# Kernel tuning notes

Measured on AMD Instinct MI355X. Metric: run time of the kernel, lower is better.

Reference implementation:

```python
import jax, jax.numpy as jnp
import numpy as np

N = 100000    # nodes
R = 8         # relations
HFR = 128     # input feature dim
HTO = 128     # output feature dim
NNZ = 1600000 # edges (nonzeros of the (N*R, N) sparse matrix)


def setup_inputs() -> dict:
    key = jax.random.key(0)
    k1, k2, k3, k4, k5 = jax.random.split(key, 5)
    nodes = jax.random.normal(k1, (N, HFR), dtype=jnp.float32)
    rows = jax.random.randint(k2, (NNZ,), 0, N * R)   # row index into (N*R, N) sparse matrix
    cols = jax.random.randint(k3, (NNZ,), 0, N)       # column = source node
    indices = jnp.stack([rows, cols]).astype(jnp.int64)
    values = jax.random.uniform(k4, (NNZ,), dtype=jnp.float32)
    # xavier-uniform-ish init for (r, hfr, hto) relation weights
    weights = jax.random.normal(k5, (R, HFR, HTO), dtype=jnp.float32) * np.float32(1.0 / np.sqrt(HFR))
    return {"nodes": nodes, "indices": indices, "values": values, "weights": weights}


def reference(nodes, indices, values, weights):
    # nodes: [n, hfr]; indices: [2, nnz]; values: [nnz]; weights: [r, hfr, hto]
    n = nodes.shape[0]
    r = weights.shape[0]
    rows, cols = indices[0], indices[1]
    # spmm: (n*r, n) sparse @ (n, hfr) dense -> (n*r, hfr)
    msgs = values[:, None] * nodes[cols]                      # [nnz, hfr] gather + scale
    agg = jax.ops.segment_sum(msgs, rows, num_segments=n * r)  # [n*r, hfr] scatter-add
    agg = agg.reshape(r, n, -1)                                # [r, n, hfr]
    # per-relation GEMM 'rij,rnj->nri' followed by sum over r, fused into one einsum
    out = jnp.einsum('rij,rnj->ni', weights, agg)              # [n, hto]
    return jax.nn.relu(out)
```

## Files before the change

### kernel.cpp

```cpp
#include <hip/hip_runtime.h>
#include <hip/hip_bf16.h>
#include <stdint.h>

#define HFR 128
#define HTO 128
#define LDN 136

typedef short short8 __attribute__((ext_vector_type(8)));
typedef float f32x4  __attribute__((ext_vector_type(4)));
typedef unsigned long long u64;

static __device__ __forceinline__ unsigned short f2bf(float x) {
    __hip_bfloat16 h = __float2bfloat16(x);
    return *reinterpret_cast<unsigned short*>(&h);
}
static __device__ __forceinline__ float bflo(unsigned int x) {
    return __uint_as_float(x << 16);
}
static __device__ __forceinline__ float bfhi(unsigned int x) {
    return __uint_as_float(x & 0xffff0000u);
}

__global__ __launch_bounds__(256) void zero_i32(int* __restrict__ p, int n) {
    int i = blockIdx.x * 256 + threadIdx.x;
    if (i < n) p[i] = 0;
}

__global__ __launch_bounds__(256)
void count_kernel(const int* __restrict__ rows, int* __restrict__ cnt,
                  int N, int nnz) {
    int e = blockIdx.x * 256 + threadIdx.x;
    if (e >= nnz) return;
    int row = rows[e];
    int r   = row / N;
    int dst = row - r * N;
    atomicAdd(&cnt[dst], 1);
}

__global__ __launch_bounds__(256)
void scan_reduce(const int* __restrict__ cnt, int* __restrict__ bsum, int N) {
    __shared__ int s[256];
    int t = threadIdx.x;
    int i = blockIdx.x * 256 + t;
    s[t] = (i < N) ? cnt[i] : 0;
    __syncthreads();
    for (int off = 128; off > 0; off >>= 1) {
        if (t < off) s[t] += s[t + off];
        __syncthreads();
    }
    if (t == 0) bsum[blockIdx.x] = s[0];
}

__global__ __launch_bounds__(1024)
void scan_block(int* __restrict__ bsum, int nb) {
    __shared__ int s[1024];
    int t = threadIdx.x;
    s[t] = (t < nb) ? bsum[t] : 0;
    __syncthreads();
    for (int off = 1; off < 1024; off <<= 1) {
        int o = (t >= off) ? s[t - off] : 0;
        __syncthreads();
        s[t] += o;
        __syncthreads();
    }
    if (t < nb) bsum[t] = (t == 0) ? 0 : s[t - 1];
}

__global__ __launch_bounds__(256)
void scan_final(int* __restrict__ cnt, const int* __restrict__ bsum, int N) {
    __shared__ int s[256];
    int t = threadIdx.x;
    int i = blockIdx.x * 256 + t;
    int v = (i < N) ? cnt[i] : 0;
    s[t] = v;
    __syncthreads();
    for (int off = 1; off < 256; off <<= 1) {
        int o = (t >= off) ? s[t - off] : 0;
        __syncthreads();
        s[t] += o;
        __syncthreads();
    }
    int ex = ((t == 0) ? 0 : s[t - 1]) + bsum[blockIdx.x];
    if (i < N) cnt[i] = ex;
}

__global__ __launch_bounds__(256, 2)
void fused_tp(const float* __restrict__ nodes,
              const float* __restrict__ weights,
              __hip_bfloat16* __restrict__ H,
              const int* __restrict__ rows, const int* __restrict__ cols,
              const float* __restrict__ vals,
              int* __restrict__ cursor, u64* __restrict__ sorted,
              int N, int R, int nnz, int Tblocks) {
    __shared__ unsigned short nd[128 * LDN];
    __shared__ unsigned short wt[128 * LDN];

    if ((int)blockIdx.x >= Tblocks) {
        int e = (blockIdx.x - Tblocks) * 256 + threadIdx.x;
        if (e >= nnz) return;
        int row = rows[e];
        int r   = row / N;
        int dst = row - r * N;
        int pos = atomicAdd(&cursor[dst], 1);
        unsigned int lo = (unsigned int)cols[e] | ((unsigned int)r << 17);
        u64 rec = ((u64)__float_as_uint(vals[e]) << 32) | (u64)lo;
        sorted[pos] = rec;
        return;
    }

    const int t    = threadIdx.x;
    const int n0   = blockIdx.x * 128;
    const int lane = t & 63;
    const int w    = t >> 6;
    const int m    = lane & 15;
    const int quad = lane >> 4;
    const int q8   = quad * 8;
    const int w32  = w * 32;

    const float4* src4 = reinterpret_cast<const float4*>(nodes);
#pragma unroll
    for (int it = 0; it < 8; ++it) {
        int id  = t + 256 * it;
        int row = id >> 4;
        int k8  = id & 15;
        float4 v0 = make_float4(0.f, 0.f, 0.f, 0.f);
        float4 v1 = v0;
        if (n0 + row < N) {
            v0 = src4[(size_t)(n0 + row) * 32 + k8 * 2];
            v1 = src4[(size_t)(n0 + row) * 32 + k8 * 2 + 1];
        }
        short8 sv;
        sv[0] = f2bf(v0.x); sv[1] = f2bf(v0.y); sv[2] = f2bf(v0.z); sv[3] = f2bf(v0.w);
        sv[4] = f2bf(v1.x); sv[5] = f2bf(v1.y); sv[6] = f2bf(v1.z); sv[7] = f2bf(v1.w);
        *reinterpret_cast<short8*>(&nd[row * LDN + k8 * 8]) = sv;
    }

    for (int r = 0; r < R; ++r) {
        __syncthreads();
        const float4* wsrc = reinterpret_cast<const float4*>(weights + (size_t)r * HFR * HTO);
#pragma unroll
        for (int it = 0; it < 8; ++it) {
            int id  = t + 256 * it;
            int row = id >> 4;
            int k8  = id & 15;
            float4 v0 = wsrc[row * 32 + k8 * 2];
            float4 v1 = wsrc[row * 32 + k8 * 2 + 1];
            short8 sv;
            sv[0] = f2bf(v0.x); sv[1] = f2bf(v0.y); sv[2] = f2bf(v0.z); sv[3] = f2bf(v0.w);
            sv[4] = f2bf(v1.x); sv[5] = f2bf(v1.y); sv[6] = f2bf(v1.z); sv[7] = f2bf(v1.w);
            *reinterpret_cast<short8*>(&wt[row * LDN + k8 * 8]) = sv;
        }
        __syncthreads();

        f32x4 acc[2][8];
#pragma unroll
        for (int t2 = 0; t2 < 2; ++t2)
#pragma unroll
            for (int j = 0; j < 8; ++j) acc[t2][j] = (f32x4)(0.f);

#pragma unroll
        for (int kk = 0; kk < HFR; kk += 32) {
            short8 a0 = *reinterpret_cast<const short8*>(&nd[(w32 +      m) * LDN + kk + q8]);
            short8 a1 = *reinterpret_cast<const short8*>(&nd[(w32 + 16 + m) * LDN + kk + q8]);
#pragma unroll
            for (int j = 0; j < 8; ++j) {
                short8 b = *reinterpret_cast<const short8*>(&wt[(j * 16 + m) * LDN + kk + q8]);
                acc[0][j] = __builtin_amdgcn_mfma_f32_16x16x32_bf16(a0, b, acc[0][j], 0, 0, 0);
                acc[1][j] = __builtin_amdgcn_mfma_f32_16x16x32_bf16(a1, b, acc[1][j], 0, 0, 0);
            }
        }

#pragma unroll
        for (int t2 = 0; t2 < 2; ++t2) {
            int rowbase = n0 + w32 + t2 * 16 + quad * 4;
#pragma unroll
            for (int reg = 0; reg < 4; ++reg) {
                int n = rowbase + reg;
                if (n < N) {
                    __hip_bfloat16* dst = H + ((size_t)r * N + n) * HTO + m;
#pragma unroll
                    for (int j = 0; j < 8; ++j)
                        dst[j * 16] = __float2bfloat16(acc[t2][j][reg]);
                }
            }
        }
    }
}

__global__ __launch_bounds__(256)
void gather_kernel(const u64* __restrict__ sorted,
                   const int* __restrict__ cursor,
                   const __hip_bfloat16* __restrict__ H,
                   float* __restrict__ out, int N) {
    const int wave = threadIdx.x >> 6;
    const int lane = threadIdx.x & 63;
    const int n = blockIdx.x * 4 + wave;
    if (n >= N) return;

    int e         = (n == 0) ? 0 : cursor[n - 1];
    const int end = cursor[n];

    float a0 = 0.f, a1 = 0.f, b0 = 0.f, b1 = 0.f;
    float c0 = 0.f, c1 = 0.f, d0 = 0.f, d1 = 0.f;

    const unsigned short* Hu = reinterpret_cast<const unsigned short*>(H);

#define HROW(q) reinterpret_cast<const unsigned int*>( \
        Hu + ((((size_t)((unsigned int)(q) >> 17) & 7) * (size_t)N + \
               ((unsigned int)(q) & 0x1FFFF)) << 7))
#define VAL(q)  __uint_as_float((unsigned int)((q) >> 32))

    for (; e + 8 <= end; e += 8) {
        const u64* p = sorted + __builtin_amdgcn_readfirstlane(e);
        u64 q0 = p[0], q1 = p[1], q2 = p[2], q3 = p[3];
        u64 q4 = p[4], q5 = p[5], q6 = p[6], q7 = p[7];
        unsigned int x0 = HROW(q0)[lane];
        unsigned int x1 = HROW(q1)[lane];
        unsigned int x2 = HROW(q2)[lane];
        unsigned int x3 = HROW(q3)[lane];
        unsigned int x4 = HROW(q4)[lane];
        unsigned int x5 = HROW(q5)[lane];
        unsigned int x6 = HROW(q6)[lane];
        unsigned int x7 = HROW(q7)[lane];
        a0 = fmaf(bflo(x0), VAL(q0), a0); a1 = fmaf(bfhi(x0), VAL(q0), a1);
        b0 = fmaf(bflo(x1), VAL(q1), b0); b1 = fmaf(bfhi(x1), VAL(q1), b1);
        c0 = fmaf(bflo(x2), VAL(q2), c0); c1 = fmaf(bfhi(x2), VAL(q2), c1);
        d0 = fmaf(bflo(x3), VAL(q3), d0); d1 = fmaf(bfhi(x3), VAL(q3), d1);
        a0 = fmaf(bflo(x4), VAL(q4), a0); a1 = fmaf(bfhi(x4), VAL(q4), a1);
        b0 = fmaf(bflo(x5), VAL(q5), b0); b1 = fmaf(bfhi(x5), VAL(q5), b1);
        c0 = fmaf(bflo(x6), VAL(q6), c0); c1 = fmaf(bfhi(x6), VAL(q6), c1);
        d0 = fmaf(bflo(x7), VAL(q7), d0); d1 = fmaf(bfhi(x7), VAL(q7), d1);
    }
    for (; e + 2 <= end; e += 2) {
        const u64* p = sorted + __builtin_amdgcn_readfirstlane(e);
        u64 q0 = p[0], q1 = p[1];
        unsigned int x0 = HROW(q0)[lane];
        unsigned int x1 = HROW(q1)[lane];
        a0 = fmaf(bflo(x0), VAL(q0), a0); a1 = fmaf(bfhi(x0), VAL(q0), a1);
        b0 = fmaf(bflo(x1), VAL(q1), b0); b1 = fmaf(bfhi(x1), VAL(q1), b1);
    }
    if (e < end) {
        u64 q0 = sorted[e];
        unsigned int x0 = HROW(q0)[lane];
        a0 = fmaf(bflo(x0), VAL(q0), a0); a1 = fmaf(bfhi(x0), VAL(q0), a1);
    }
#undef HROW
#undef VAL

    float2 o;
    o.x = fmaxf(a0 + b0 + c0 + d0, 0.f);
    o.y = fmaxf(a1 + b1 + c1 + d1, 0.f);
    *reinterpret_cast<float2*>(out + (size_t)n * HTO + lane * 2) = o;
}

extern "C" void kernel_launch(void* const* d_in, const int* in_sizes, int n_in,
                              void* d_out, int out_size, void* d_ws, size_t ws_size,
                              hipStream_t stream) {
    const float* nodes   = (const float*)d_in[0];
    const int*   indices = (const int*)d_in[1];
    const float* vals    = (const float*)d_in[2];
    const float* weights = (const float*)d_in[3];

    const int N   = in_sizes[0] / HFR;
    const int nnz = in_sizes[1] / 2;
    const int R   = in_sizes[3] / (HFR * HTO);

    const int* rows = indices;
    const int* cols = indices + nnz;

    char* ws = (char*)d_ws;
    __hip_bfloat16* H = (__hip_bfloat16*)ws;
    size_t off = (size_t)R * N * HTO * sizeof(__hip_bfloat16);
    u64* sorted = (u64*)(ws + off);
    off += (size_t)nnz * sizeof(u64);
    int* cnt = (int*)(ws + off);
    off += (size_t)N * sizeof(int);
    int* bsum = (int*)(ws + off);

    float* out = (float*)d_out;

    const int NB = (N + 255) / 256;
    const int Tblocks = (N + 127) / 128;
    const int Pblocks = (nnz + 255) / 256;

    zero_i32<<<NB, 256, 0, stream>>>(cnt, N);
    count_kernel<<<Pblocks, 256, 0, stream>>>(rows, cnt, N, nnz);
    scan_reduce<<<NB, 256, 0, stream>>>(cnt, bsum, N);
    scan_block<<<1, 1024, 0, stream>>>(bsum, NB);
    scan_final<<<NB, 256, 0, stream>>>(cnt, bsum, N);
    fused_tp<<<Tblocks + Pblocks, 256, 0, stream>>>(nodes, weights, H,
                                                    rows, cols, vals,
                                                    cnt, sorted, N, R, nnz, Tblocks);
    gather_kernel<<<(N + 3) / 4, 256, 0, stream>>>(sorted, cnt, H, out, N);
}
```

Measured before the change: 382.9 us.

## Pre-swizzle bf16 weights into MFMA fragment layout and read B directly from global

Adds a small pre-pass kernel that converts fp32 relation weights to bf16 and stores them in the exact per-lane MFMA B-fragment order. The transform kernel then reads B fragments straight from global/L2 instead of converting and staging each relation's weights into shared memory, which removes the per-relation LDS fill and two barriers per relation. Halving LDS use lets launch bounds ask for 4 blocks per CU. The trade-off is that every wave now issues repeated global loads for B, relying on cache hits. There is also a fallback that places the swizzled weights at the tail of the output buffer when workspace is short, before gather overwrites it.

```diff
diff --git a/kernel.cpp b/kernel.cpp
--- a/kernel.cpp
+++ b/kernel.cpp
@@ -84,16 +84,30 @@
     if (i < N) cnt[i] = ex;
 }
 
-__global__ __launch_bounds__(256, 2)
+__global__ __launch_bounds__(256)
+void conv_weights(const float* __restrict__ weights, short8* __restrict__ Wf) {
+    int id = blockIdx.x * 256 + threadIdx.x;
+    int lane = id & 63;
+    int kk   = (id >> 6) & 3;
+    int j    = (id >> 8) & 7;
+    int r    = id >> 11;
+    int m = lane & 15, q = lane >> 4;
+    const float* src = weights + (((size_t)r * HFR) + j * 16 + m) * HTO + kk * 32 + q * 8;
+    short8 sv;
+#pragma unroll
+    for (int e = 0; e < 8; ++e) sv[e] = f2bf(src[e]);
+    Wf[((r * 4 + kk) * 8 + j) * 64 + lane] = sv;
+}
+
+__global__ __launch_bounds__(256, 4)
 void fused_tp(const float* __restrict__ nodes,
-              const float* __restrict__ weights,
+              const short8* __restrict__ Wf,
               __hip_bfloat16* __restrict__ H,
               const int* __restrict__ rows, const int* __restrict__ cols,
               const float* __restrict__ vals,
               int* __restrict__ cursor, u64* __restrict__ sorted,
               int N, int R, int nnz, int Tblocks) {
     __shared__ unsigned short nd[128 * LDN];
-    __shared__ unsigned short wt[128 * LDN];
 
     if ((int)blockIdx.x >= Tblocks) {
         int e = (blockIdx.x - Tblocks) * 256 + threadIdx.x;
@@ -134,23 +148,10 @@
         sv[4] = f2bf(v1.x); sv[5] = f2bf(v1.y); sv[6] = f2bf(v1.z); sv[7] = f2bf(v1.w);
         *reinterpret_cast<short8*>(&nd[row * LDN + k8 * 8]) = sv;
     }
+    __syncthreads();
 
     for (int r = 0; r < R; ++r) {
-        __syncthreads();
-        const float4* wsrc = reinterpret_cast<const float4*>(weights + (size_t)r * HFR * HTO);
-#pragma unroll
-        for (int it = 0; it < 8; ++it) {
-            int id  = t + 256 * it;
-            int row = id >> 4;
-            int k8  = id & 15;
-            float4 v0 = wsrc[row * 32 + k8 * 2];
-            float4 v1 = wsrc[row * 32 + k8 * 2 + 1];
-            short8 sv;
-            sv[0] = f2bf(v0.x); sv[1] = f2bf(v0.y); sv[2] = f2bf(v0.z); sv[3] = f2bf(v0.w);
-            sv[4] = f2bf(v1.x); sv[5] = f2bf(v1.y); sv[6] = f2bf(v1.z); sv[7] = f2bf(v1.w);
-            *reinterpret_cast<short8*>(&wt[row * LDN + k8 * 8]) = sv;
-        }
-        __syncthreads();
+        const short8* wr = Wf + (size_t)r * 2048 + lane;
 
         f32x4 acc[2][8];
 #pragma unroll
@@ -159,12 +160,12 @@
             for (int j = 0; j < 8; ++j) acc[t2][j] = (f32x4)(0.f);
 
 #pragma unroll
-        for (int kk = 0; kk < HFR; kk += 32) {
-            short8 a0 = *reinterpret_cast<const short8*>(&nd[(w32 +      m) * LDN + kk + q8]);
-            short8 a1 = *reinterpret_cast<const short8*>(&nd[(w32 + 16 + m) * LDN + kk + q8]);
+        for (int kk = 0; kk < 4; ++kk) {
+            short8 a0 = *reinterpret_cast<const short8*>(&nd[(w32 +      m) * LDN + kk * 32 + q8]);
+            short8 a1 = *reinterpret_cast<const short8*>(&nd[(w32 + 16 + m) * LDN + kk * 32 + q8]);
 #pragma unroll
             for (int j = 0; j < 8; ++j) {
-                short8 b = *reinterpret_cast<const short8*>(&wt[(j * 16 + m) * LDN + kk + q8]);
+                short8 b = wr[kk * 512 + j * 64];
                 acc[0][j] = __builtin_amdgcn_mfma_f32_16x16x32_bf16(a0, b, acc[0][j], 0, 0, 0);
                 acc[1][j] = __builtin_amdgcn_mfma_f32_16x16x32_bf16(a1, b, acc[1][j], 0, 0, 0);
             }
@@ -276,6 +277,15 @@
     int* cnt = (int*)(ws + off);
     off += (size_t)N * sizeof(int);
     int* bsum = (int*)(ws + off);
+    off += 1024 * sizeof(int);
+
+    const size_t WFBYTES = (size_t)R * 4 * 8 * 64 * sizeof(short8);
+    short8* Wf;
+    if (off + WFBYTES <= ws_size) {
+        Wf = (short8*)(ws + off);
+    } else {
+        Wf = (short8*)((char*)d_out + (size_t)out_size - WFBYTES);
+    }
 
     float* out = (float*)d_out;
 
@@ -283,12 +293,13 @@
     const int Tblocks = (N + 127) / 128;
     const int Pblocks = (nnz + 255) / 256;
 
+    conv_weights<<<(R * 4 * 8 * 64) / 256, 256, 0, stream>>>(weights, Wf);
     zero_i32<<<NB, 256, 0, stream>>>(cnt, N);
     count_kernel<<<Pblocks, 256, 0, stream>>>(rows, cnt, N, nnz);
     scan_reduce<<<NB, 256, 0, stream>>>(cnt, bsum, N);
     scan_block<<<1, 1024, 0, stream>>>(bsum, NB);
     scan_final<<<NB, 256, 0, stream>>>(cnt, bsum, N);
-    fused_tp<<<Tblocks + Pblocks, 256, 0, stream>>>(nodes, weights, H,
+    fused_tp<<<Tblocks + Pblocks, 256, 0, stream>>>(nodes, Wf, H,
                                                     rows, cols, vals,
                                                     cnt, sorted, N, R, nnz, Tblocks);
     gather_kernel<<<(N + 3) / 4, 256, 0, stream>>>(sorted, cnt, H, out, N);
```

Measured after the change: 378.8 us. About the same (-1.1%).
